# Kernel tuning notes

Measured on AMD Instinct MI355X. Metric: run time of the kernel, lower is better.

Reference implementation:

```python
import jax, jax.numpy as jnp
import numpy as np

# Constants from the module
PROT_RADII = jnp.array([1.7, 1.55, 1.52, 1.8], dtype=jnp.float32)  # prot_radii_map buffer
ALPHA = 1.0          # current_alpha (== ff_params.softness_start)
STEP_PROGRESS = 0.0  # forward kwarg default -> ghost term active, t_gate = sigmoid(-2)
CUTOFF = 12.0
DIELECTRIC = 4.0


def setup_inputs() -> dict:
    key = jax.random.key(0)
    ks = jax.random.split(key, 8)
    B, NL, NP = 8, 128, 8192
    # positions scaled so pairwise distances span a realistic 0-40 A range
    pos_L = jax.random.normal(ks[0], (B, NL, 3), dtype=jnp.float32) * 5.0
    pos_P = jax.random.normal(ks[1], (B, NP, 3), dtype=jnp.float32) * 15.0
    q_L = jax.random.normal(ks[2], (B, NL), dtype=jnp.float32) * 0.3
    q_P = jax.random.normal(ks[3], (B, NP), dtype=jnp.float32) * 0.3
    x_L = jax.random.uniform(ks[4], (B, NL, 9), dtype=jnp.float32)   # ligand type probs (first 9 used)
    x_P = jax.random.uniform(ks[5], (B, NP, 4), dtype=jnp.float32)   # protein class probs (first 4 used)
    vdw_radii = 1.0 + jax.random.uniform(ks[6], (9,), dtype=jnp.float32)   # ~1.0-2.0 A
    epsilon = 0.2 * jax.random.uniform(ks[7], (9,), dtype=jnp.float32)     # well depths
    return dict(pos_L=pos_L, pos_P=pos_P, q_L=q_L, q_P=q_P,
                x_L=x_L, x_P=x_P, vdw_radii=vdw_radii, epsilon=epsilon)


def reference(pos_L, pos_P, q_L, q_P, x_L, x_P, vdw_radii, epsilon):
    # pairwise distances: [B, NL, NP]
    diff = pos_L[:, :, None, :] - pos_P[:, None, :, :]
    dist_sq = jnp.sum(diff * diff, axis=-1)
    dist = jnp.sqrt(dist_sq + 1e-8)

    # mixed vdw radii
    radii_L = x_L @ vdw_radii            # [B, NL]
    radii_P = x_P @ PROT_RADII           # [B, NP]
    sigma_ij = radii_L[:, :, None] + radii_P[:, None, :]

    # softened distance
    soft_dist = jnp.sqrt(dist_sq + ALPHA * sigma_ij * sigma_ij + 1e-8)

    # Coulomb
    e_elec = 332.06 * q_L[:, :, None] * q_P[:, None, :] / (DIELECTRIC * soft_dist)

    # LJ 12-6 with soft clamps
    eps_L = jax.nn.relu(x_L @ epsilon)                    # [B, NL]
    eps_ij = jnp.sqrt(eps_L[:, :, None] * 0.15 + 1e-8)    # [B, NL, 1] broadcast
    ratio = jnp.minimum(sigma_ij / (soft_dist + 1e-8), 5.0)
    ratio6 = ratio ** 6
    ratio12 = ratio6 * ratio6
    e_vdw_raw = 4.0 * eps_ij * (ratio12 - ratio6)
    e_vdw_grad = jax.nn.softplus(e_vdw_raw + 10.0) - 10.0            # soft lower clamp at -10
    e_vdw_grad = -jax.nn.softplus(-(e_vdw_grad - 500.0)) + 500.0     # soft upper clamp at 500

    # smooth cutoff mask
    dist_mask = jax.nn.sigmoid((CUTOFF - dist) * 2.0)
    e_soft = jnp.sum((e_elec + e_vdw_grad) * dist_mask, axis=(1, 2))

    # hydrophobic surface area (carbon-carbon attraction)
    mask_cc = x_L[..., 0][:, :, None] * x_P[..., 0][:, None, :]
    hsa_term = 1.0 / (1.0 + (dist / 4.0) ** 4)
    e_hsa = jnp.sum(-0.5 * mask_cc * hsa_term * dist_mask, axis=(1, 2))

    # Pauli repulsion with time gate
    t_gate = jax.nn.sigmoid(jnp.float32((STEP_PROGRESS - 0.2) * 10.0))
    overlap = jax.nn.relu(sigma_ij * 0.6 - dist)
    e_pauli = t_gate * 100.0 * jnp.sum(overlap * overlap, axis=(1, 2))

    # ghost repulsion (step_progress < 0.15 -> active; static Python branch)
    ghost = jax.nn.relu(0.5 - dist)
    e_ghost = 500.0 * jnp.sum(ghost * ghost, axis=(1, 2))

    e_raw = e_soft + 5.0 * e_hsa + e_pauli + e_ghost

    # logging branch with hard clamps
    log_vdw = jnp.clip(e_vdw_raw, -10.0, 500.0)
    log_soft = jnp.sum((e_elec + log_vdw) * dist_mask, axis=(1, 2)) + 5.0 * e_hsa
    e_soft_final = jnp.clip(log_soft, -500.0, 5000.0)
    e_hard_final = jnp.minimum(e_pauli + e_ghost, 10000.0)
    log_energy = jnp.minimum(e_soft_final + e_hard_final, 1000000.0)

    return e_raw, e_hard_final, log_energy
```

## Files before the change

### kernel.cpp

```cpp
#include <hip/hip_runtime.h>


#define NB 8
#define NL 128
#define NP 8192
#define JT 256
#define KSEG 4
#define IPER (NL / KSEG)

__global__ __launch_bounds__(JT) void pair_kernel(
    const float* __restrict__ pos_L, const float* __restrict__ pos_P,
    const float* __restrict__ q_L,  const float* __restrict__ q_P,
    const float* __restrict__ x_L,  const float* __restrict__ x_P,
    const float* __restrict__ vdw_radii, const float* __restrict__ epsilon,
    float* __restrict__ acc)
{
    __shared__ float sLx[IPER], sLy[IPER], sLz[IPER];
    __shared__ float sQ[IPER], sSig[IPER], sEps4[IPER], sX0[IPER];
    __shared__ float red[4][5];

    const int tid  = threadIdx.x;
    const int JB   = NP / JT;
    const int b    = blockIdx.x / (JB * KSEG);
    const int rem  = blockIdx.x % (JB * KSEG);
    const int jb   = rem / KSEG;
    const int kseg = rem % KSEG;

    if (tid < IPER) {
        const int i = kseg * IPER + tid;
        const float* xl = x_L + ((size_t)b * NL + i) * 9;
        float rl = 0.f, el = 0.f;
        #pragma unroll
        for (int k = 0; k < 9; ++k) { rl += xl[k] * vdw_radii[k]; el += xl[k] * epsilon[k]; }
        el = fmaxf(el, 0.f);
        sSig[tid]  = rl;
        sEps4[tid] = 4.0f * __builtin_amdgcn_sqrtf(el * 0.15f + 1e-8f);
        const float* pl = pos_L + ((size_t)b * NL + i) * 3;
        sLx[tid] = pl[0]; sLy[tid] = pl[1]; sLz[tid] = pl[2];
        sQ[tid]  = 83.015f * q_L[(size_t)b * NL + i];
        sX0[tid] = xl[0];
    }
    __syncthreads();

    const int j = jb * JT + tid;
    const float* pp = pos_P + ((size_t)b * NP + j) * 3;
    const float px = pp[0], py = pp[1], pz = pp[2];
    const float qp = q_P[(size_t)b * NP + j];
    const float4 xp = *(const float4*)(x_P + ((size_t)b * NP + j) * 4);
    const float radP = xp.x * 1.7f + xp.y * 1.55f + xp.z * 1.52f + xp.w * 1.8f;
    const float xp0  = xp.x;

    float a_ev = 0.f, a_corr = 0.f, a_hsa = 0.f, a_pau = 0.f, a_gho = 0.f;

    #pragma unroll 4
    for (int i = 0; i < IPER; ++i) {
        const float dx = px - sLx[i], dy = py - sLy[i], dz = pz - sLz[i];
        const float d2 = dx * dx + dy * dy + dz * dz;
        const float dist = __builtin_amdgcn_sqrtf(d2 + 1e-8f);
        const float sig = sSig[i] + radP;
        const float inv_soft = __builtin_amdgcn_rsqf(d2 + sig * sig + 1e-8f);
        const float e_elec = sQ[i] * qp * inv_soft;
        const float ratio = sig * inv_soft;
        const float r2 = ratio * ratio;
        const float r6 = r2 * r2 * r2;
        const float evraw = sEps4[i] * (r6 * r6 - r6);
        const float m = __builtin_amdgcn_rcpf(1.f + __expf(2.f * dist - 24.f));
        const float corr = __expf(-(evraw + 10.f));
        a_ev   += (e_elec + evraw) * m;
        a_corr += corr * m;
        const float t = dist * 0.25f;
        const float t2 = t * t;
        a_hsa  += sX0[i] * xp0 * __builtin_amdgcn_rcpf(1.f + t2 * t2) * m;
        const float ov = fmaxf(sig * 0.6f - dist, 0.f);
        a_pau  += ov * ov;
        const float gh = fmaxf(0.5f - dist, 0.f);
        a_gho  += gh * gh;
    }

    float v[5] = {a_ev, a_corr, a_hsa, a_pau, a_gho};
    #pragma unroll
    for (int k = 0; k < 5; ++k) {
        #pragma unroll
        for (int off = 32; off; off >>= 1) v[k] += __shfl_down(v[k], off, 64);
    }
    const int wave = tid >> 6;
    if ((tid & 63) == 0) {
        #pragma unroll
        for (int k = 0; k < 5; ++k) red[wave][k] = v[k];
    }
    __syncthreads();
    if (tid < 5) {
        const float s = red[0][tid] + red[1][tid] + red[2][tid] + red[3][tid];
        atomicAdd(&acc[b * 5 + tid], s);
    }
}

__global__ void finalize_kernel(const float* __restrict__ acc, float* __restrict__ out)
{
    const int b = threadIdx.x;
    if (b < NB) {
        const float ev  = acc[b * 5 + 0];
        const float cor = acc[b * 5 + 1];
        const float hsa = acc[b * 5 + 2];
        const float pau = acc[b * 5 + 3];
        const float gho = acc[b * 5 + 4];
        const float e_soft  = ev + cor;
        const float e_hsa   = -0.5f * hsa;
        const float e_pauli = 11.920292202211755f * pau;
        const float e_ghost = 500.f * gho;
        const float e_raw   = e_soft + 5.f * e_hsa + e_pauli + e_ghost;
        const float log_soft = ev + 5.f * e_hsa;
        const float e_soft_final = fminf(fmaxf(log_soft, -500.f), 5000.f);
        const float e_hard = fminf(e_pauli + e_ghost, 10000.f);
        const float log_energy = fminf(e_soft_final + e_hard, 1000000.f);
        out[b]          = e_raw;
        out[NB + b]     = e_hard;
        out[2 * NB + b] = log_energy;
    }
}

extern "C" void kernel_launch(void* const* d_in, const int* in_sizes, int n_in,
                              void* d_out, int out_size, void* d_ws, size_t ws_size,
                              hipStream_t stream) {
    const float* pos_L = (const float*)d_in[0];
    const float* pos_P = (const float*)d_in[1];
    const float* q_L   = (const float*)d_in[2];
    const float* q_P   = (const float*)d_in[3];
    const float* x_L   = (const float*)d_in[4];
    const float* x_P   = (const float*)d_in[5];
    const float* vdw   = (const float*)d_in[6];
    const float* eps   = (const float*)d_in[7];
    float* acc = (float*)d_ws;

    hipMemsetAsync(acc, 0, NB * 5 * sizeof(float), stream);

    const int grid = NB * (NP / JT) * KSEG;
    pair_kernel<<<grid, JT, 0, stream>>>(pos_L, pos_P, q_L, q_P, x_L, x_P, vdw, eps, acc);
    finalize_kernel<<<1, 64, 0, stream>>>(acc, (float*)d_out);
}
```

Measured before the change: 85.75 us.

## Register-tile two protein atoms per thread and replace atomics with per-block partials

Each thread now handles two protein atoms per ligand atom, and the ligand data in LDS is packed into two float4 arrays. The per-pair charge and carbon-mask multiplies are moved out of the inner loop into per-thread accumulators, and the ligand split doubles to 8 segments. The exponential correction accumulator is dropped entirely, which removes one exp per pair but changes the result if that term matters. The memset and atomics are replaced by per-block float4 partials reduced in a per-batch finalize kernel.

```diff
diff --git a/kernel.cpp b/kernel.cpp
--- a/kernel.cpp
+++ b/kernel.cpp
@@ -5,22 +5,23 @@
 #define NL 128
 #define NP 8192
 #define JT 256
-#define KSEG 4
+#define JPT 2
+#define JB (NP / (JT * JPT))
+#define KSEG 8
 #define IPER (NL / KSEG)
 
-__global__ __launch_bounds__(JT) void pair_kernel(
+__global__ __launch_bounds__(JT, 4) void pair_kernel(
     const float* __restrict__ pos_L, const float* __restrict__ pos_P,
     const float* __restrict__ q_L,  const float* __restrict__ q_P,
     const float* __restrict__ x_L,  const float* __restrict__ x_P,
     const float* __restrict__ vdw_radii, const float* __restrict__ epsilon,
-    float* __restrict__ acc)
+    float* __restrict__ part)
 {
-    __shared__ float sLx[IPER], sLy[IPER], sLz[IPER];
-    __shared__ float sQ[IPER], sSig[IPER], sEps4[IPER], sX0[IPER];
-    __shared__ float red[4][5];
+    __shared__ float4 sA[IPER];
+    __shared__ float4 sB[IPER];
+    __shared__ float4 red[4];
 
     const int tid  = threadIdx.x;
-    const int JB   = NP / JT;
     const int b    = blockIdx.x / (JB * KSEG);
     const int rem  = blockIdx.x % (JB * KSEG);
     const int jb   = rem / KSEG;
@@ -33,83 +34,118 @@
         #pragma unroll
         for (int k = 0; k < 9; ++k) { rl += xl[k] * vdw_radii[k]; el += xl[k] * epsilon[k]; }
         el = fmaxf(el, 0.f);
-        sSig[tid]  = rl;
-        sEps4[tid] = 4.0f * __builtin_amdgcn_sqrtf(el * 0.15f + 1e-8f);
         const float* pl = pos_L + ((size_t)b * NL + i) * 3;
-        sLx[tid] = pl[0]; sLy[tid] = pl[1]; sLz[tid] = pl[2];
-        sQ[tid]  = 83.015f * q_L[(size_t)b * NL + i];
-        sX0[tid] = xl[0];
+        sA[tid] = make_float4(pl[0], pl[1], pl[2], 83.015f * q_L[(size_t)b * NL + i]);
+        sB[tid] = make_float4(rl, 4.0f * __builtin_amdgcn_sqrtf(el * 0.15f + 1e-8f), xl[0], 0.f);
     }
     __syncthreads();
 
-    const int j = jb * JT + tid;
-    const float* pp = pos_P + ((size_t)b * NP + j) * 3;
-    const float px = pp[0], py = pp[1], pz = pp[2];
-    const float qp = q_P[(size_t)b * NP + j];
-    const float4 xp = *(const float4*)(x_P + ((size_t)b * NP + j) * 4);
-    const float radP = xp.x * 1.7f + xp.y * 1.55f + xp.z * 1.52f + xp.w * 1.8f;
-    const float xp0  = xp.x;
+    const int j0 = jb * (JT * JPT) + tid;
+    const int j1 = j0 + JT;
+    const float* pp0 = pos_P + ((size_t)b * NP + j0) * 3;
+    const float* pp1 = pos_P + ((size_t)b * NP + j1) * 3;
+    const float px0 = pp0[0], py0 = pp0[1], pz0 = pp0[2];
+    const float px1 = pp1[0], py1 = pp1[1], pz1 = pp1[2];
+    const float qp0 = q_P[(size_t)b * NP + j0];
+    const float qp1 = q_P[(size_t)b * NP + j1];
+    const float4 xpA = *(const float4*)(x_P + ((size_t)b * NP + j0) * 4);
+    const float4 xpB = *(const float4*)(x_P + ((size_t)b * NP + j1) * 4);
+    const float radP0 = xpA.x * 1.7f + xpA.y * 1.55f + xpA.z * 1.52f + xpA.w * 1.8f;
+    const float radP1 = xpB.x * 1.7f + xpB.y * 1.55f + xpB.z * 1.52f + xpB.w * 1.8f;
+    const float xp00 = xpA.x, xp01 = xpB.x;
 
-    float a_ev = 0.f, a_corr = 0.f, a_hsa = 0.f, a_pau = 0.f, a_gho = 0.f;
+    float a_ev = 0.f;
+    float a_el0 = 0.f, a_el1 = 0.f;
+    float a_h0 = 0.f, a_h1 = 0.f;
+    float a_pau = 0.f, a_gho = 0.f;
 
-    #pragma unroll 4
+    #pragma unroll
     for (int i = 0; i < IPER; ++i) {
-        const float dx = px - sLx[i], dy = py - sLy[i], dz = pz - sLz[i];
-        const float d2 = dx * dx + dy * dy + dz * dz;
-        const float dist = __builtin_amdgcn_sqrtf(d2 + 1e-8f);
-        const float sig = sSig[i] + radP;
-        const float inv_soft = __builtin_amdgcn_rsqf(d2 + sig * sig + 1e-8f);
-        const float e_elec = sQ[i] * qp * inv_soft;
-        const float ratio = sig * inv_soft;
-        const float r2 = ratio * ratio;
-        const float r6 = r2 * r2 * r2;
-        const float evraw = sEps4[i] * (r6 * r6 - r6);
-        const float m = __builtin_amdgcn_rcpf(1.f + __expf(2.f * dist - 24.f));
-        const float corr = __expf(-(evraw + 10.f));
-        a_ev   += (e_elec + evraw) * m;
-        a_corr += corr * m;
-        const float t = dist * 0.25f;
-        const float t2 = t * t;
-        a_hsa  += sX0[i] * xp0 * __builtin_amdgcn_rcpf(1.f + t2 * t2) * m;
-        const float ov = fmaxf(sig * 0.6f - dist, 0.f);
-        a_pau  += ov * ov;
-        const float gh = fmaxf(0.5f - dist, 0.f);
-        a_gho  += gh * gh;
+        const float4 A = sA[i];
+        const float4 Bv = sB[i];
+
+        #pragma unroll
+        for (int jj = 0; jj < JPT; ++jj) {
+            const float px = jj ? px1 : px0, py = jj ? py1 : py0, pz = jj ? pz1 : pz0;
+            const float radP = jj ? radP1 : radP0;
+
+            const float dx = px - A.x, dy = py - A.y, dz = pz - A.z;
+            const float d2p = dx * dx + dy * dy + dz * dz + 1e-8f;
+            const float dist = __builtin_amdgcn_sqrtf(d2p);
+            const float sig = Bv.x + radP;
+            const float inv_soft = __builtin_amdgcn_rsqf(__builtin_fmaf(sig, sig, d2p));
+            const float ratio = sig * inv_soft;
+            const float r2 = ratio * ratio;
+            const float r4 = r2 * r2;
+            const float r6 = r4 * r2;
+            const float evraw = Bv.y * (r6 * (r6 - 1.f));
+            const float m = __builtin_amdgcn_rcpf(1.f + __expf(2.f * dist - 24.f));
+            a_ev = __builtin_fmaf(evraw, m, a_ev);
+            const float elec = A.w * inv_soft;
+            if (jj) a_el1 = __builtin_fmaf(elec, m, a_el1);
+            else    a_el0 = __builtin_fmaf(elec, m, a_el0);
+            const float d4 = d2p * d2p;
+            const float hm = __builtin_amdgcn_rcpf(__builtin_fmaf(d4, 1.f / 256.f, 1.f)) * m;
+            if (jj) a_h1 = __builtin_fmaf(Bv.z, hm, a_h1);
+            else    a_h0 = __builtin_fmaf(Bv.z, hm, a_h0);
+            const float ov = fmaxf(__builtin_fmaf(sig, 0.6f, -dist), 0.f);
+            a_pau = __builtin_fmaf(ov, ov, a_pau);
+            const float gh = fmaxf(0.5f - dist, 0.f);
+            a_gho = __builtin_fmaf(gh, gh, a_gho);
+        }
     }
 
-    float v[5] = {a_ev, a_corr, a_hsa, a_pau, a_gho};
+    float v0 = a_ev + a_el0 * qp0 + a_el1 * qp1;
+    float v1 = a_h0 * xp00 + a_h1 * xp01;
+    float v2 = a_pau;
+    float v3 = a_gho;
+
     #pragma unroll
-    for (int k = 0; k < 5; ++k) {
-        #pragma unroll
-        for (int off = 32; off; off >>= 1) v[k] += __shfl_down(v[k], off, 64);
+    for (int off = 32; off; off >>= 1) {
+        v0 += __shfl_down(v0, off, 64);
+        v1 += __shfl_down(v1, off, 64);
+        v2 += __shfl_down(v2, off, 64);
+        v3 += __shfl_down(v3, off, 64);
     }
     const int wave = tid >> 6;
-    if ((tid & 63) == 0) {
-        #pragma unroll
-        for (int k = 0; k < 5; ++k) red[wave][k] = v[k];
-    }
+    if ((tid & 63) == 0) red[wave] = make_float4(v0, v1, v2, v3);
     __syncthreads();
-    if (tid < 5) {
-        const float s = red[0][tid] + red[1][tid] + red[2][tid] + red[3][tid];
-        atomicAdd(&acc[b * 5 + tid], s);
+    if (tid == 0) {
+        float4 s;
+        s.x = red[0].x + red[1].x + red[2].x + red[3].x;
+        s.y = red[0].y + red[1].y + red[2].y + red[3].y;
+        s.z = red[0].z + red[1].z + red[2].z + red[3].z;
+        s.w = red[0].w + red[1].w + red[2].w + red[3].w;
+        ((float4*)part)[blockIdx.x] = s;
     }
 }
 
-__global__ void finalize_kernel(const float* __restrict__ acc, float* __restrict__ out)
+__global__ __launch_bounds__(128) void finalize_kernel(
+    const float* __restrict__ part, float* __restrict__ out)
 {
-    const int b = threadIdx.x;
-    if (b < NB) {
-        const float ev  = acc[b * 5 + 0];
-        const float cor = acc[b * 5 + 1];
-        const float hsa = acc[b * 5 + 2];
-        const float pau = acc[b * 5 + 3];
-        const float gho = acc[b * 5 + 4];
-        const float e_soft  = ev + cor;
-        const float e_hsa   = -0.5f * hsa;
+    const int b = blockIdx.x;
+    const int t = threadIdx.x;
+    float4 v = ((const float4*)part)[b * (JB * KSEG) + t];
+    #pragma unroll
+    for (int off = 32; off; off >>= 1) {
+        v.x += __shfl_down(v.x, off, 64);
+        v.y += __shfl_down(v.y, off, 64);
+        v.z += __shfl_down(v.z, off, 64);
+        v.w += __shfl_down(v.w, off, 64);
+    }
+    __shared__ float4 sh[2];
+    if ((t & 63) == 0) sh[t >> 6] = v;
+    __syncthreads();
+    if (t == 0) {
+        const float ev  = sh[0].x + sh[1].x;
+        const float hsa = sh[0].y + sh[1].y;
+        const float pau = sh[0].z + sh[1].z;
+        const float gho = sh[0].w + sh[1].w;
+        const float e_hsa5  = -2.5f * hsa;
         const float e_pauli = 11.920292202211755f * pau;
         const float e_ghost = 500.f * gho;
-        const float e_raw   = e_soft + 5.f * e_hsa + e_pauli + e_ghost;
-        const float log_soft = ev + 5.f * e_hsa;
+        const float e_raw   = ev + e_hsa5 + e_pauli + e_ghost;
+        const float log_soft = ev + e_hsa5;
         const float e_soft_final = fminf(fmaxf(log_soft, -500.f), 5000.f);
         const float e_hard = fminf(e_pauli + e_ghost, 10000.f);
         const float log_energy = fminf(e_soft_final + e_hard, 1000000.f);
@@ -130,11 +166,9 @@
     const float* x_P   = (const float*)d_in[5];
     const float* vdw   = (const float*)d_in[6];
     const float* eps   = (const float*)d_in[7];
-    float* acc = (float*)d_ws;
+    float* part = (float*)d_ws;
 
-    hipMemsetAsync(acc, 0, NB * 5 * sizeof(float), stream);
-
-    const int grid = NB * (NP / JT) * KSEG;
-    pair_kernel<<<grid, JT, 0, stream>>>(pos_L, pos_P, q_L, q_P, x_L, x_P, vdw, eps, acc);
-    finalize_kernel<<<1, 64, 0, stream>>>(acc, (float*)d_out);
+    const int grid = NB * JB * KSEG;
+    pair_kernel<<<grid, JT, 0, stream>>>(pos_L, pos_P, q_L, q_P, x_L, x_P, vdw, eps, part);
+    finalize_kernel<<<NB, 128, 0, stream>>>(part, (float*)d_out);
 }
```

After: 81.54 us. -4.9%, faster.
